# Kernel optimization log

Hardware: AMD Instinct MI355X
Metric: run time of the kernel (lower is better)

The kernel has to match this reference:

```python
import jax, jax.numpy as jnp
import numpy as np

NUM_CAV = 62000            # CAVs in the ragged batch
K = 3                      # past frames per object


def _counts():
    # deterministic ragged counts in [1, 31]; sum = 2000 * 496 = 992000 objects
    return ((np.arange(NUM_CAV) % 31) + 1).astype(np.int32)


def setup_inputs() -> dict:
    key = jax.random.key(0)
    k1, k2 = jax.random.split(key)
    counts = _counts()
    n_obj = int(counts.sum())  # 992000
    # [N, 3, 7] past 7-dof boxes; only [..., :2] (x, y) is used
    past_k_object_bbx = jax.random.normal(k1, (n_obj, K, 7), dtype=jnp.float32) * 10.0
    # strictly increasing timestamps per CAV so frame-to-frame dt != 0
    dt = jax.random.uniform(k2, (NUM_CAV, K), dtype=jnp.float32, minval=0.05, maxval=0.2)
    past_k_time_interval = jnp.cumsum(dt, axis=1).reshape(-1)  # flat, view(-1,3) compatible
    past_k_object_cav_num = jnp.asarray(counts)
    return {
        'past_k_object_bbx': past_k_object_bbx,
        'past_k_time_interval': past_k_time_interval,
        'past_k_object_cav_num': past_k_object_cav_num,
    }


def reference(past_k_object_bbx, past_k_time_interval, past_k_object_cav_num):
    # Faithful vectorization of extract_date_backup1 (j-indexed replicate loop ==
    # repeat_interleave of per-CAV time rows to per-object rows).
    n_obj = past_k_object_bbx.shape[0]
    # time grid per CAV, reversed so index -1 is the most recent frame
    td = jnp.flip(past_k_time_interval.reshape(-1, K), axis=1)        # [C, 3]
    coords = jnp.flip(past_k_object_bbx[:, :, :2], axis=1)           # [N, 3, 2]
    coords = coords - coords[:, -1:, :]                               # normalize to last frame
    # ragged row replication -> gather via cumulative offsets
    offsets = jnp.cumsum(past_k_object_cav_num)                       # [C]
    cav_idx = jnp.searchsorted(offsets, jnp.arange(n_obj), side='right')
    td_rep = td[cav_idx]                                              # [N, 3]
    td_norm = td_rep - td_rep[:, -1:]                                  # [N, 3]
    dt = td_rep[:, 1:] - td_rep[:, :-1]                                # [N, 2] (time_encode)
    distance = coords[:, 1:, :] - coords[:, :-1, :]                    # [N, 2, 2]
    speed = distance / dt[..., None]                                   # [N, 2, 2]
    obj_input = jnp.concatenate([distance, speed], axis=-1)[None]      # [1, N, 2, 4]
    # linear extrapolation of last motion to t = 0 (the 'query')
    last_len = td_norm[:, -1] - td_norm[:, -2]                          # [N]
    safe_len = jnp.where(last_len == 0, jnp.float32(1.0), last_len)
    extrap = coords[:, -1, :] + (coords[:, -1, :] - coords[:, -2, :]) * (-td_rep[:, -1:]) / safe_len[:, None]
    query = jnp.where((last_len == 0)[:, None], jnp.float32(0.0), extrap).reshape(1, n_obj, 1, 2)
    target_time_diff = -td_rep[:, -1]                                  # [N]
    time_encode = dt                                                   # [N, 2]
    return obj_input, query, time_encode, target_time_diff
```

## Files before the change

### kernel.cpp

```cpp
#include <hip/hip_runtime.h>
#include <stdint.h>

#define SCAN_BS 1024
#define OBJ_BS  256
#define SLAB_F  (OBJ_BS * 21)
#define SLAB_CH (SLAB_F / 256)

__device__ __forceinline__ void gload_lds16(const void* g, void* l) {
    __builtin_amdgcn_global_load_lds(
        (const __attribute__((address_space(1))) uint32_t*)g,
        (__attribute__((address_space(3))) uint32_t*)l, 16, 0, 0);
}


__global__ __launch_bounds__(SCAN_BS) void scan_scatter_kernel(
    const int* __restrict__ counts, int C,
    int* __restrict__ cavIdx) {

    __shared__ int sdata[SCAN_BS];
    __shared__ int wsum[SCAN_BS / 64];

    const int tid  = threadIdx.x;
    const int lane = tid & 63;
    const int wid  = tid >> 6;
    const int b    = blockIdx.x;
    const int gid  = b * SCAN_BS + tid;
    const int chunkStart = b * SCAN_BS;

    const int v = (gid < C) ? counts[gid] : 0;
    sdata[tid] = v;

    int csum = 0;
    for (int idx = tid; idx < chunkStart; idx += SCAN_BS) csum += counts[idx];
    #pragma unroll
    for (int o = 32; o > 0; o >>= 1) csum += __shfl_down(csum, o, 64);
    if (lane == 0) wsum[wid] = csum;
    __syncthreads();

    for (int ofs = 1; ofs < SCAN_BS; ofs <<= 1) {
        int add = (tid >= ofs) ? sdata[tid - ofs] : 0;
        __syncthreads();
        sdata[tid] += add;
        __syncthreads();
    }

    int carry = 0;
    #pragma unroll
    for (int w = 0; w < SCAN_BS / 64; ++w) carry += wsum[w];

    if (gid < C) {
        const int end   = sdata[tid] + carry;
        const int start = end - v;
        for (int s = start; s < end; ++s) cavIdx[s] = gid;
    }
}


__global__ __launch_bounds__(OBJ_BS) void motion_kernel(
    const float* __restrict__ bbx, const float* __restrict__ tint,
    const int* __restrict__ cavIdx, int N,
    float* __restrict__ out) {

    __shared__ __align__(16) float sb[SLAB_F];

    const int tid  = threadIdx.x;
    const int lane = tid & 63;
    const int wid  = tid >> 6;
    const long long blockStart = (long long)blockIdx.x * OBJ_BS;
    const int nObjBlk = (int)min((long long)OBJ_BS, (long long)N - blockStart);

    const float* gsrc = bbx + blockStart * 21;
    if (nObjBlk == OBJ_BS) {
        #pragma unroll
        for (int ch = wid; ch < SLAB_CH; ch += 4)
            gload_lds16((const void*)(gsrc + ch * 256 + lane * 4), (void*)(sb + ch * 256));
    } else {
        const int nElem = nObjBlk * 21;
        for (int k = tid; k < nElem; k += OBJ_BS) sb[k] = gsrc[k];
    }

    const int i = (int)(blockStart + tid);
    const bool act = (tid < nObjBlk);

    const int   cav = act ? cavIdx[i] : 0;
    const float t0  = tint[3 * cav + 0];
    const float t1  = tint[3 * cav + 1];
    const float t2  = tint[3 * cav + 2];

    __syncthreads();

    if (!act) return;

    const float dt0 = t1 - t2;
    const float dt1 = t0 - t1;

    const float* bp = sb + tid * 21;
    const float x0 = bp[0],  y0 = bp[1];
    const float x1 = bp[7],  y1 = bp[8];
    const float x2 = bp[14], y2 = bp[15];

    const float c0x = x2 - x0, c0y = y2 - y0;
    const float c1x = x1 - x0, c1y = y1 - y0;

    const float d0x = c1x - c0x, d0y = c1y - c0y;
    const float d1x = 0.0f - c1x, d1y = 0.0f - c1y;

    const float s0x = d0x / dt0, s0y = d0y / dt0;
    const float s1x = d1x / dt1, s1y = d1y / dt1;

    const float last_len = 0.0f - (t1 - t0);
    const float safe_len = (last_len == 0.0f) ? 1.0f : last_len;
    const float exx = ((0.0f - c1x) * (0.0f - t0)) / safe_len;
    const float exy = ((0.0f - c1y) * (0.0f - t0)) / safe_len;
    const float qx = (last_len == 0.0f) ? 0.0f : exx;
    const float qy = (last_len == 0.0f) ? 0.0f : exy;

    const size_t Ns = (size_t)N;
    float4* oi = (float4*)out;
    oi[(size_t)i * 2 + 0] = make_float4(d0x, d0y, s0x, s0y);
    oi[(size_t)i * 2 + 1] = make_float4(d1x, d1y, s1x, s1y);

    float2* q  = (float2*)(out + 8 * Ns);
    q[i] = make_float2(qx, qy);

    float2* te = (float2*)(out + 10 * Ns);
    te[i] = make_float2(dt0, dt1);

    out[12 * Ns + (size_t)i] = 0.0f - t0;
}


extern "C" void kernel_launch(void* const* d_in, const int* in_sizes, int n_in,
                              void* d_out, int out_size, void* d_ws, size_t ws_size,
                              hipStream_t stream) {
    const float* bbx  = (const float*)d_in[0];
    const float* tint = (const float*)d_in[1];
    const int*   cnt  = (const int*)d_in[2];
    float* out = (float*)d_out;

    const int N = in_sizes[0] / 21;
    const int C = in_sizes[2];

    const int nb  = (C + SCAN_BS - 1) / SCAN_BS;
    const int nob = (N + OBJ_BS - 1) / OBJ_BS;

    int* cavIdx = (int*)d_ws;

    scan_scatter_kernel<<<nb, SCAN_BS, 0, stream>>>(cnt, C, cavIdx);
    motion_kernel<<<nob, OBJ_BS, 0, stream>>>(bbx, tint, cavIdx, N, out);
}
```

Measured before the change: 41.76 us.

## Use wave-shuffle scan with smaller blocks and grid-stride direct-load motion kernel

```diff
diff --git a/kernel.cpp b/kernel.cpp
--- a/kernel.cpp
+++ b/kernel.cpp
@@ -1,132 +1,104 @@
 #include <hip/hip_runtime.h>
 #include <stdint.h>
 
-#define SCAN_BS 1024
-#define OBJ_BS  256
-#define SLAB_F  (OBJ_BS * 21)
-#define SLAB_CH (SLAB_F / 256)
-
-__device__ __forceinline__ void gload_lds16(const void* g, void* l) {
-    __builtin_amdgcn_global_load_lds(
-        (const __attribute__((address_space(1))) uint32_t*)g,
-        (__attribute__((address_space(3))) uint32_t*)l, 16, 0, 0);
-}
+#define SCAN_BS 256
+#define MOT_BS  256
 
 
 __global__ __launch_bounds__(SCAN_BS) void scan_scatter_kernel(
-    const int* __restrict__ counts, int C,
-    int* __restrict__ cavIdx) {
+    const int* __restrict__ counts, int C, int* __restrict__ cavIdx) {
 
-    __shared__ int sdata[SCAN_BS];
-    __shared__ int wsum[SCAN_BS / 64];
+    __shared__ int cw[SCAN_BS / 64];
+    __shared__ int wv[SCAN_BS / 64];
 
     const int tid  = threadIdx.x;
     const int lane = tid & 63;
     const int wid  = tid >> 6;
-    const int b    = blockIdx.x;
-    const int gid  = b * SCAN_BS + tid;
-    const int chunkStart = b * SCAN_BS;
+    const int gid  = blockIdx.x * SCAN_BS + tid;
+    const int chunkStart = blockIdx.x * SCAN_BS;
 
     const int v = (gid < C) ? counts[gid] : 0;
-    sdata[tid] = v;
 
     int csum = 0;
     for (int idx = tid; idx < chunkStart; idx += SCAN_BS) csum += counts[idx];
     #pragma unroll
     for (int o = 32; o > 0; o >>= 1) csum += __shfl_down(csum, o, 64);
-    if (lane == 0) wsum[wid] = csum;
+
+    int inc = v;
+    #pragma unroll
+    for (int o = 1; o < 64; o <<= 1) {
+        int t = __shfl_up(inc, o, 64);
+        if (lane >= o) inc += t;
+    }
+
+    if (lane == 0)  cw[wid] = csum;
+    if (lane == 63) wv[wid] = inc;
     __syncthreads();
 
-    for (int ofs = 1; ofs < SCAN_BS; ofs <<= 1) {
-        int add = (tid >= ofs) ? sdata[tid - ofs] : 0;
-        __syncthreads();
-        sdata[tid] += add;
-        __syncthreads();
+    int base = 0;
+    #pragma unroll
+    for (int w = 0; w < SCAN_BS / 64; ++w) {
+        base += cw[w];
+        if (w < wid) base += wv[w];
     }
 
-    int carry = 0;
-    #pragma unroll
-    for (int w = 0; w < SCAN_BS / 64; ++w) carry += wsum[w];
-
     if (gid < C) {
-        const int end   = sdata[tid] + carry;
+        const int end   = base + inc;
         const int start = end - v;
         for (int s = start; s < end; ++s) cavIdx[s] = gid;
     }
 }
 
 
-__global__ __launch_bounds__(OBJ_BS) void motion_kernel(
+__global__ __launch_bounds__(MOT_BS) void motion_kernel(
     const float* __restrict__ bbx, const float* __restrict__ tint,
-    const int* __restrict__ cavIdx, int N,
-    float* __restrict__ out) {
+    const int* __restrict__ cavIdx, int N, float* __restrict__ out) {
 
-    __shared__ __align__(16) float sb[SLAB_F];
+    const int stride = gridDim.x * MOT_BS;
+    const size_t Ns = (size_t)N;
 
-    const int tid  = threadIdx.x;
-    const int lane = tid & 63;
-    const int wid  = tid >> 6;
-    const long long blockStart = (long long)blockIdx.x * OBJ_BS;
-    const int nObjBlk = (int)min((long long)OBJ_BS, (long long)N - blockStart);
+    for (int i = blockIdx.x * MOT_BS + threadIdx.x; i < N; i += stride) {
+        const int cav = cavIdx[i];
+        const float t0 = tint[3 * cav + 0];
+        const float t1 = tint[3 * cav + 1];
+        const float t2 = tint[3 * cav + 2];
 
-    const float* gsrc = bbx + blockStart * 21;
-    if (nObjBlk == OBJ_BS) {
-        #pragma unroll
-        for (int ch = wid; ch < SLAB_CH; ch += 4)
-            gload_lds16((const void*)(gsrc + ch * 256 + lane * 4), (void*)(sb + ch * 256));
-    } else {
-        const int nElem = nObjBlk * 21;
-        for (int k = tid; k < nElem; k += OBJ_BS) sb[k] = gsrc[k];
+        const float* bp = bbx + (size_t)i * 21;
+        const float x0 = bp[0],  y0 = bp[1];
+        const float x1 = bp[7],  y1 = bp[8];
+        const float x2 = bp[14], y2 = bp[15];
+
+        const float dt0 = t1 - t2;
+        const float dt1 = t0 - t1;
+
+        const float c0x = x2 - x0, c0y = y2 - y0;
+        const float c1x = x1 - x0, c1y = y1 - y0;
+
+        const float d0x = c1x - c0x, d0y = c1y - c0y;
+        const float d1x = 0.0f - c1x, d1y = 0.0f - c1y;
+
+        const float s0x = d0x / dt0, s0y = d0y / dt0;
+        const float s1x = d1x / dt1, s1y = d1y / dt1;
+
+        const float last_len = 0.0f - (t1 - t0);
+        const float safe_len = (last_len == 0.0f) ? 1.0f : last_len;
+        const float exx = ((0.0f - c1x) * (0.0f - t0)) / safe_len;
+        const float exy = ((0.0f - c1y) * (0.0f - t0)) / safe_len;
+        const float qx = (last_len == 0.0f) ? 0.0f : exx;
+        const float qy = (last_len == 0.0f) ? 0.0f : exy;
+
+        float4* oi = (float4*)out;
+        oi[(size_t)i * 2 + 0] = make_float4(d0x, d0y, s0x, s0y);
+        oi[(size_t)i * 2 + 1] = make_float4(d1x, d1y, s1x, s1y);
+
+        float2* q  = (float2*)(out + 8 * Ns);
+        q[i] = make_float2(qx, qy);
+
+        float2* te = (float2*)(out + 10 * Ns);
+        te[i] = make_float2(dt0, dt1);
+
+        out[12 * Ns + (size_t)i] = 0.0f - t0;
     }
-
-    const int i = (int)(blockStart + tid);
-    const bool act = (tid < nObjBlk);
-
-    const int   cav = act ? cavIdx[i] : 0;
-    const float t0  = tint[3 * cav + 0];
-    const float t1  = tint[3 * cav + 1];
-    const float t2  = tint[3 * cav + 2];
-
-    __syncthreads();
-
-    if (!act) return;
-
-    const float dt0 = t1 - t2;
-    const float dt1 = t0 - t1;
-
-    const float* bp = sb + tid * 21;
-    const float x0 = bp[0],  y0 = bp[1];
-    const float x1 = bp[7],  y1 = bp[8];
-    const float x2 = bp[14], y2 = bp[15];
-
-    const float c0x = x2 - x0, c0y = y2 - y0;
-    const float c1x = x1 - x0, c1y = y1 - y0;
-
-    const float d0x = c1x - c0x, d0y = c1y - c0y;
-    const float d1x = 0.0f - c1x, d1y = 0.0f - c1y;
-
-    const float s0x = d0x / dt0, s0y = d0y / dt0;
-    const float s1x = d1x / dt1, s1y = d1y / dt1;
-
-    const float last_len = 0.0f - (t1 - t0);
-    const float safe_len = (last_len == 0.0f) ? 1.0f : last_len;
-    const float exx = ((0.0f - c1x) * (0.0f - t0)) / safe_len;
-    const float exy = ((0.0f - c1y) * (0.0f - t0)) / safe_len;
-    const float qx = (last_len == 0.0f) ? 0.0f : exx;
-    const float qy = (last_len == 0.0f) ? 0.0f : exy;
-
-    const size_t Ns = (size_t)N;
-    float4* oi = (float4*)out;
-    oi[(size_t)i * 2 + 0] = make_float4(d0x, d0y, s0x, s0y);
-    oi[(size_t)i * 2 + 1] = make_float4(d1x, d1y, s1x, s1y);
-
-    float2* q  = (float2*)(out + 8 * Ns);
-    q[i] = make_float2(qx, qy);
-
-    float2* te = (float2*)(out + 10 * Ns);
-    te[i] = make_float2(dt0, dt1);
-
-    out[12 * Ns + (size_t)i] = 0.0f - t0;
 }
 
 
@@ -141,11 +113,12 @@
     const int N = in_sizes[0] / 21;
     const int C = in_sizes[2];
 
-    const int nb  = (C + SCAN_BS - 1) / SCAN_BS;
-    const int nob = (N + OBJ_BS - 1) / OBJ_BS;
+    const int nb = (C + SCAN_BS - 1) / SCAN_BS;
+    int nob = (N + MOT_BS - 1) / MOT_BS;
+    if (nob > 2048) nob = 2048;
 
     int* cavIdx = (int*)d_ws;
 
     scan_scatter_kernel<<<nb, SCAN_BS, 0, stream>>>(cnt, C, cavIdx);
-    motion_kernel<<<nob, OBJ_BS, 0, stream>>>(bbx, tint, cavIdx, N, out);
+    motion_kernel<<<nob, MOT_BS, 0, stream>>>(bbx, tint, cavIdx, N, out);
 }
```

Result: slower. 60.75 us (+45.5%).
